# Optimization experiments

Measured on AMD Instinct MI355X. Metric: run time of the kernel, lower is better.

Reference implementation:

```python
import jax, jax.numpy as jnp
import numpy as np

TNEI = 2
TOPK = 4
NEIGH = 2 * TNEI + 1  # window size = 5


def _normalize(x, eps=1e-12):
    # matches torch F.normalize(dim=-1)
    n = jnp.linalg.norm(x, axis=-1, keepdims=True)
    return x / jnp.maximum(n, eps)


def setup_inputs() -> dict:
    key = jax.random.key(0)
    ks = jax.random.split(key, 10)
    B, T, C = 32, 256, 128
    x = jax.random.normal(ks[0], (B, T, C), jnp.float32)
    radj = jax.random.randint(ks[1], (B, T, T), 0, 2).astype(jnp.int32)
    inxs = jax.random.randint(ks[2], (B, T, TOPK), 0, T)
    s = 1.0 / np.sqrt(C)
    W_pf = jax.random.normal(ks[3], (C, C), jnp.float32) * s
    W_ns = jax.random.normal(ks[4], (C, C), jnp.float32) * s
    W_v = jax.random.normal(ks[5], (C, C), jnp.float32) * s
    v_pf = jax.random.normal(ks[6], (NEIGH,), jnp.float32)
    g_pf = jnp.linalg.norm(v_pf)[None]  # weight_norm gain, shape (1,)
    v_ns = jax.random.normal(ks[7], (TOPK,), jnp.float32)
    g_ns = jnp.linalg.norm(v_ns)[None]
    return dict(x=x, radj=radj, inxs=inxs, W_pf=W_pf, W_ns=W_ns, W_v=W_v,
                v_pf=v_pf, g_pf=g_pf, v_ns=v_ns, g_ns=g_ns)


def reference(x, radj, inxs, W_pf, W_ns, W_v, v_pf, g_pf, v_ns, g_ns):
    B, T, C = x.shape
    pf = _normalize(x @ W_pf.T)
    ns = _normalize(x @ W_ns.T)
    v = x @ W_v.T
    # windowed neighbor indices, identical to _tneigh_mask(mode='all')
    i = jnp.arange(T)
    start = jnp.clip(i - TNEI, 0, T - NEIGH)
    nbr = start[:, None] + jnp.arange(NEIGH)[None, :]  # (T, NEIGH)
    ctx = pf[:, nbr]  # (B, T, NEIGH, C) — replaces one-hot ctxinx einsum
    # pairwise window similarity: (B,T,T,n,n)
    sim = jnp.einsum('bxic,byjc->bxyij', ctx, ctx)
    # AdaptiveMaxPool2d((n,1)) == max over the last (key-window) axis
    sim_pf = sim.max(axis=-1)  # (B,T,T,n)
    w_pf = g_pf[0] * v_pf / jnp.linalg.norm(v_pf)  # weight-norm agg_pf
    sim_pf = jnp.einsum('bxyi,i->bxy', sim_pf, w_pf)
    # topk-neighbor branch: inxs gathers ns rows (replaces one-hot einsum)
    ns_q = ns[jnp.arange(B)[:, None, None], inxs]  # (B,T,TOPK,C)
    sim_ns = jnp.einsum('bxnc,byc->bxyn', ns_q, ns)  # (B,T,T,TOPK)
    w_ns = g_ns[0] * v_ns / jnp.linalg.norm(v_ns)  # weight-norm agg_ns
    sim_ns = jnp.einsum('bxyn,n->bxy', sim_ns, w_ns)
    # adjacency mask: 0 -> -1e22, >0 -> 0
    mask = jnp.where(radj == 0, jnp.float32(-1e22), jnp.float32(0.0))
    attn = jax.nn.softmax(sim_pf + sim_ns + mask, axis=-1)  # (B,T,T)
    return jnp.einsum('bkt,btd->bkd', attn, v)  # (B,T,C)
```

## Files before the change

kernel.cpp:

```cpp
#include <hip/hip_runtime.h>
#include <math.h>


#define TT 256
#define CC 128

using bf16x8 = __attribute__((ext_vector_type(8))) short;
using f32x4  = __attribute__((ext_vector_type(4))) float;

__device__ __forceinline__ short bf_hi(float x) {
    unsigned u = __float_as_uint(x);
    return (short)((u + 0x7FFFu + ((u >> 16) & 1u)) >> 16);
}
__device__ __forceinline__ void bf_split(float x, short& h, short& l) {
    h = bf_hi(x);
    float hf = __uint_as_float(((unsigned)(unsigned short)h) << 16);
    l = bf_hi(x - hf);
}
__device__ __forceinline__ float max5(float a, float b, float c, float d, float e) {
    return fmaxf(fmaxf(fmaxf(a, b), fmaxf(c, d)), e);
}

__global__ __launch_bounds__(256, 4) void proj_kernel(
    const float* __restrict__ x,
    const float* __restrict__ W0, const float* __restrict__ W1, const float* __restrict__ W2,
    float* __restrict__ pf, float* __restrict__ ns,
    short* __restrict__ vt_h, short* __restrict__ vt_l)
{
    __shared__ short Ah[32 * 40], Al[32 * 40];
    __shared__ short Bh[128 * 40], Bl[128 * 40];
    __shared__ float ssb[32][4];
    const int tid = threadIdx.x;
    const int row0 = blockIdx.x * 32;
    const int m = blockIdx.y;
    const float* __restrict__ W = (m == 0) ? W0 : (m == 1) ? W1 : W2;
    const int lane = tid & 63, wn = tid >> 6;
    const int quad = lane >> 4, lr = lane & 15;
    f32x4 z4 = {0.f, 0.f, 0.f, 0.f};
    f32x4 acc[2][2] = {{z4, z4}, {z4, z4}};

    for (int k0 = 0; k0 < CC; k0 += 32) {
        __syncthreads();
        {
            int r = tid >> 3, q = (tid & 7) * 4;
            float4 a4 = *(const float4*)&x[(row0 + r) * CC + k0 + q];
            short4 h4, l4;
            bf_split(a4.x, h4.x, l4.x); bf_split(a4.y, h4.y, l4.y);
            bf_split(a4.z, h4.z, l4.z); bf_split(a4.w, h4.w, l4.w);
            *(short4*)&Ah[r * 40 + q] = h4; *(short4*)&Al[r * 40 + q] = l4;
        }
        for (int i = 0; i < 4; i++) {
            int flat = i * 256 + tid, r = flat >> 3, q = (flat & 7) * 4;
            float4 b4 = *(const float4*)&W[r * CC + k0 + q];
            short4 h4, l4;
            bf_split(b4.x, h4.x, l4.x); bf_split(b4.y, h4.y, l4.y);
            bf_split(b4.z, h4.z, l4.z); bf_split(b4.w, h4.w, l4.w);
            *(short4*)&Bh[r * 40 + q] = h4; *(short4*)&Bl[r * 40 + q] = l4;
        }
        __syncthreads();
        bf16x8 ah[2], al[2], bh[2], bl[2];
        for (int ra = 0; ra < 2; ra++) {
            int ar = (16 * ra + lr) * 40 + quad * 8;
            ah[ra] = *(bf16x8*)&Ah[ar];
            al[ra] = *(bf16x8*)&Al[ar];
        }
        for (int tn = 0; tn < 2; tn++) {
            int br = (32 * wn + 16 * tn + lr) * 40 + quad * 8;
            bh[tn] = *(bf16x8*)&Bh[br];
            bl[tn] = *(bf16x8*)&Bl[br];
        }
        for (int ra = 0; ra < 2; ra++)
            for (int tn = 0; tn < 2; tn++) {
                acc[ra][tn] = __builtin_amdgcn_mfma_f32_16x16x32_bf16(ah[ra], bh[tn], acc[ra][tn], 0, 0, 0);
                acc[ra][tn] = __builtin_amdgcn_mfma_f32_16x16x32_bf16(ah[ra], bl[tn], acc[ra][tn], 0, 0, 0);
                acc[ra][tn] = __builtin_amdgcn_mfma_f32_16x16x32_bf16(al[ra], bh[tn], acc[ra][tn], 0, 0, 0);
            }
    }
    if (m < 2) {
        float* __restrict__ o = (m == 0) ? pf : ns;
        float ssp[2][4];
        for (int ra = 0; ra < 2; ra++)
            for (int reg = 0; reg < 4; reg++) {
                float s = acc[ra][0][reg] * acc[ra][0][reg]
                        + acc[ra][1][reg] * acc[ra][1][reg];
                for (int off = 1; off < 16; off <<= 1) s += __shfl_xor(s, off);
                ssp[ra][reg] = s;
            }
        if (lr == 0)
            for (int ra = 0; ra < 2; ra++)
                for (int reg = 0; reg < 4; reg++)
                    ssb[16 * ra + quad * 4 + reg][wn] = ssp[ra][reg];
        __syncthreads();
        for (int ra = 0; ra < 2; ra++)
            for (int reg = 0; reg < 4; reg++) {
                int ml = 16 * ra + quad * 4 + reg;
                float ss = ssb[ml][0] + ssb[ml][1] + ssb[ml][2] + ssb[ml][3];
                float inv = 1.f / fmaxf(sqrtf(ss), 1e-12f);
                int row = row0 + ml;
                for (int tn = 0; tn < 2; tn++)
                    o[row * CC + 32 * wn + 16 * tn + lr] = acc[ra][tn][reg] * inv;
            }
    } else {
        for (int ra = 0; ra < 2; ra++) {
            int rowbase = row0 + 16 * ra + quad * 4;
            int b = rowbase >> 8, t0 = rowbase & 255;
            for (int tn = 0; tn < 2; tn++) {
                int c = 32 * wn + 16 * tn + lr;
                short4 h4, l4;
                for (int reg = 0; reg < 4; reg++)
                    bf_split(acc[ra][tn][reg], ((short*)&h4)[reg], ((short*)&l4)[reg]);
                size_t o = ((size_t)b * CC + c) * TT + t0;
                *(short4*)&vt_h[o] = h4;
                *(short4*)&vt_l[o] = l4;
            }
        }
    }
}

__global__ __launch_bounds__(256, 4) void gram_mfma(
    const float* __restrict__ pf, const float* __restrict__ ns,
    const int* __restrict__ inxs, const float* __restrict__ v_ns,
    const float* __restrict__ g_ns, float* __restrict__ G, float* __restrict__ S)
{
    __shared__ short Ah[64 * 40], Al[64 * 40], Bh[64 * 40], Bl[64 * 40];
    const int tid = threadIdx.x;
    const int m0 = blockIdx.x * 64, n0 = blockIdx.y * 64;
    const int b = blockIdx.z >> 1, half = blockIdx.z & 1;
    const float* __restrict__ Pb = pf + (size_t)b * TT * CC;
    const float* __restrict__ Nb = ns + (size_t)b * TT * CC;
    const float* __restrict__ Bsrc = half ? Nb : Pb;

    float w0 = 0.f, w1 = 0.f, w2 = 0.f, w3 = 0.f;
    int4 id0 = {0, 0, 0, 0}, id1 = {0, 0, 0, 0};
    if (half) {
        float n2 = v_ns[0]*v_ns[0] + v_ns[1]*v_ns[1] + v_ns[2]*v_ns[2] + v_ns[3]*v_ns[3];
        float sc = g_ns[0] / sqrtf(n2);
        w0 = sc*v_ns[0]; w1 = sc*v_ns[1]; w2 = sc*v_ns[2]; w3 = sc*v_ns[3];
        id0 = *(const int4*)&inxs[(b * TT + m0 + (tid >> 3)) * 4];
        id1 = *(const int4*)&inxs[(b * TT + m0 + 32 + (tid >> 3)) * 4];
    }

    const int lane = tid & 63, wave = tid >> 6;
    const int wm = wave >> 1, wn = wave & 1;
    const int quad = lane >> 4, lr = lane & 15;
    f32x4 z4 = {0.f, 0.f, 0.f, 0.f};
    f32x4 acc[2][2] = {{z4, z4}, {z4, z4}};

    for (int k0 = 0; k0 < CC; k0 += 32) {
        __syncthreads();
        for (int i = 0; i < 2; i++) {
            int flat = i * 256 + tid, r = flat >> 3, q = (flat & 7) * 4;
            float4 a4;
            if (!half) {
                a4 = *(const float4*)&Pb[(m0 + r) * CC + k0 + q];
            } else {
                int4 id = i ? id1 : id0;
                float4 aa = *(const float4*)&Nb[id.x * CC + k0 + q];
                float4 ab = *(const float4*)&Nb[id.y * CC + k0 + q];
                float4 ac = *(const float4*)&Nb[id.z * CC + k0 + q];
                float4 ad = *(const float4*)&Nb[id.w * CC + k0 + q];
                a4.x = w0*aa.x + w1*ab.x + w2*ac.x + w3*ad.x;
                a4.y = w0*aa.y + w1*ab.y + w2*ac.y + w3*ad.y;
                a4.z = w0*aa.z + w1*ab.z + w2*ac.z + w3*ad.z;
                a4.w = w0*aa.w + w1*ab.w + w2*ac.w + w3*ad.w;
            }
            float4 b4 = *(const float4*)&Bsrc[(n0 + r) * CC + k0 + q];
            short4 h4, l4;
            bf_split(a4.x, h4.x, l4.x); bf_split(a4.y, h4.y, l4.y);
            bf_split(a4.z, h4.z, l4.z); bf_split(a4.w, h4.w, l4.w);
            *(short4*)&Ah[r * 40 + q] = h4; *(short4*)&Al[r * 40 + q] = l4;
            bf_split(b4.x, h4.x, l4.x); bf_split(b4.y, h4.y, l4.y);
            bf_split(b4.z, h4.z, l4.z); bf_split(b4.w, h4.w, l4.w);
            *(short4*)&Bh[r * 40 + q] = h4; *(short4*)&Bl[r * 40 + q] = l4;
        }
        __syncthreads();
        bf16x8 bh[2], bl[2];
        for (int tn = 0; tn < 2; tn++) {
            int br = (32 * wn + 16 * tn + lr) * 40 + quad * 8;
            bh[tn] = *(bf16x8*)&Bh[br];
            bl[tn] = *(bf16x8*)&Bl[br];
        }
        for (int tm = 0; tm < 2; tm++) {
            int ar = (32 * wm + 16 * tm + lr) * 40 + quad * 8;
            bf16x8 ah = *(bf16x8*)&Ah[ar];
            bf16x8 al = *(bf16x8*)&Al[ar];
            for (int tn = 0; tn < 2; tn++) {
                acc[tm][tn] = __builtin_amdgcn_mfma_f32_16x16x32_bf16(ah, bh[tn], acc[tm][tn], 0, 0, 0);
                acc[tm][tn] = __builtin_amdgcn_mfma_f32_16x16x32_bf16(ah, bl[tn], acc[tm][tn], 0, 0, 0);
                acc[tm][tn] = __builtin_amdgcn_mfma_f32_16x16x32_bf16(al, bh[tn], acc[tm][tn], 0, 0, 0);
            }
        }
    }
    float* __restrict__ Cb = (half ? S : G) + (size_t)b * TT * TT;
    for (int tm = 0; tm < 2; tm++)
        for (int tn = 0; tn < 2; tn++) {
            int rb = m0 + 32 * wm + 16 * tm + quad * 4;
            int cb = n0 + 32 * wn + 16 * tn + lr;
            for (int reg = 0; reg < 4; reg++)
                Cb[(size_t)(rb + reg) * TT + cb] = acc[tm][tn][reg];
        }
}

__global__ __launch_bounds__(256, 2) void fused_smax_pv(
    const float* __restrict__ G, const float* __restrict__ S,
    const int* __restrict__ radj, const float* __restrict__ v_pf,
    const float* __restrict__ g_pf,
    const short* __restrict__ vt_h, const short* __restrict__ vt_l,
    float* __restrict__ out)
{
    __shared__ float Gs[20 * 256];
    __shared__ float RM[20 * 256];
    __shared__ short ATH[16 * 264];
    __shared__ short ATL[16 * 264];
    __shared__ float RD[64];
    __shared__ float RMX[64];
    const int tid = threadIdx.x;
    const int xt = blockIdx.x, b = blockIdx.y;
    const int x0 = xt * 16;
    const int rbase = min(max(x0 - 2, 0), TT - 5);
    for (int i = 0; i < 5; i++) {
        int flat = i * 256 + tid, ri = flat >> 6, q = (flat & 63) * 4;
        int r = min(rbase + ri, TT - 1);
        *(float4*)&Gs[ri * 256 + q] = *(const float4*)&G[(size_t)b * TT * TT + r * TT + q];
    }
    float n2 = 0.f;
    for (int i = 0; i < 5; i++) n2 += v_pf[i] * v_pf[i];
    float sc = g_pf[0] / sqrtf(n2);
    float wpf[5];
    for (int i = 0; i < 5; i++) wpf[i] = sc * v_pf[i];
    __syncthreads();
    for (int t = 0; t < 5; t++) {
        int task = t * 256 + tid;
        int i = task >> 6, g = task & 63;
        const float* row = &Gs[i * 256];
        float4 X = *(float4*)&row[4 * g];
        float m0_, m1_, m2_, m3_;
        if (g == 0) {
            float4 N = *(float4*)&row[4];
            float mx = fmaxf(fmaxf(X.x, X.y), fmaxf(X.z, X.w));
            m0_ = m1_ = m2_ = fmaxf(mx, N.x);
            m3_ = max5(X.y, X.z, X.w, N.x, N.y);
        } else if (g == 63) {
            float4 P = *(float4*)&row[248];
            m0_ = max5(P.z, P.w, X.x, X.y, X.z);
            float mx = fmaxf(fmaxf(X.x, X.y), fmaxf(X.z, X.w));
            m1_ = m2_ = m3_ = fmaxf(P.w, mx);
        } else {
            float4 P = *(float4*)&row[4 * g - 4];
            float4 N = *(float4*)&row[4 * g + 4];
            m0_ = max5(P.z, P.w, X.x, X.y, X.z);
            m1_ = max5(P.w, X.x, X.y, X.z, X.w);
            m2_ = max5(X.x, X.y, X.z, X.w, N.x);
            m3_ = max5(X.y, X.z, X.w, N.x, N.y);
        }
        float4 o4 = {m0_, m1_, m2_, m3_};
        *(float4*)&RM[i * 256 + 4 * g] = o4;
    }
    __syncthreads();
    const int y = tid;
    const size_t sb = (size_t)b * TT * TT;
    float lv[16];
    if (xt > 0 && xt < 15) {
        float rm[20];
        #pragma unroll
        for (int r = 0; r < 20; r++) rm[r] = RM[r * 256 + y];
        #pragma unroll
        for (int xi = 0; xi < 16; xi++) {
            float s = wpf[0] * rm[xi];
            #pragma unroll
            for (int i = 1; i < 5; i++) s = fmaf(wpf[i], rm[xi + i], s);
            lv[xi] = s;
        }
    } else {
        for (int xi = 0; xi < 16; xi++) {
            int sxr = min(max(x0 + xi - 2, 0), TT - 5) - rbase;
            float s = 0.f;
            for (int i = 0; i < 5; i++) s = fmaf(wpf[i], RM[(sxr + i) * 256 + y], s);
            lv[xi] = s;
        }
    }
    for (int xi = 0; xi < 16; xi++) {
        lv[xi] += S[sb + (x0 + xi) * TT + y];
        if (radj[sb + (x0 + xi) * TT + y] == 0) lv[xi] += -1e22f;
    }
    const int lane = tid & 63, wv = tid >> 6;
    for (int xi = 0; xi < 16; xi++) {
        float v = lv[xi];
        for (int o = 32; o; o >>= 1) v = fmaxf(v, __shfl_xor(v, o));
        if (lane == 0) RMX[xi * 4 + wv] = v;
    }
    __syncthreads();
    for (int xi = 0; xi < 16; xi++) {
        float mx = fmaxf(fmaxf(RMX[xi * 4], RMX[xi * 4 + 1]),
                         fmaxf(RMX[xi * 4 + 2], RMX[xi * 4 + 3]));
        float e = __expf(lv[xi] - mx);
        short h, l;
        bf_split(e, h, l);
        ATH[xi * 264 + y] = h;
        ATL[xi * 264 + y] = l;
        for (int o = 32; o; o >>= 1) e += __shfl_xor(e, o);
        if (lane == 0) RD[xi * 4 + wv] = e;
    }
    __syncthreads();
    const int quad = lane >> 4, lr = lane & 15;
    const int c0 = wv * 32;
    const short* __restrict__ vhb = vt_h + (size_t)b * CC * TT;
    const short* __restrict__ vlb = vt_l + (size_t)b * CC * TT;
    const int ar0 = (c0 + lr) * TT, ar1 = ar0 + 16 * TT;
    f32x4 z4 = {0.f, 0.f, 0.f, 0.f};
    f32x4 acc[2] = {z4, z4};
    #pragma unroll
    for (int k0 = 0; k0 < TT; k0 += 32) {
        int ko = k0 + quad * 8;
        bf16x8 bh = *(bf16x8*)&ATH[lr * 264 + ko];
        bf16x8 bl = *(bf16x8*)&ATL[lr * 264 + ko];
        bf16x8 a0h = *(const bf16x8*)&vhb[ar0 + ko];
        bf16x8 a0l = *(const bf16x8*)&vlb[ar0 + ko];
        bf16x8 a1h = *(const bf16x8*)&vhb[ar1 + ko];
        bf16x8 a1l = *(const bf16x8*)&vlb[ar1 + ko];
        acc[0] = __builtin_amdgcn_mfma_f32_16x16x32_bf16(a0h, bh, acc[0], 0, 0, 0);
        acc[0] = __builtin_amdgcn_mfma_f32_16x16x32_bf16(a0h, bl, acc[0], 0, 0, 0);
        acc[0] = __builtin_amdgcn_mfma_f32_16x16x32_bf16(a0l, bh, acc[0], 0, 0, 0);
        acc[1] = __builtin_amdgcn_mfma_f32_16x16x32_bf16(a1h, bh, acc[1], 0, 0, 0);
        acc[1] = __builtin_amdgcn_mfma_f32_16x16x32_bf16(a1h, bl, acc[1], 0, 0, 0);
        acc[1] = __builtin_amdgcn_mfma_f32_16x16x32_bf16(a1l, bh, acc[1], 0, 0, 0);
    }
    float sm = RD[lr * 4] + RD[lr * 4 + 1] + RD[lr * 4 + 2] + RD[lr * 4 + 3];
    float rinv = 1.f / sm;
    for (int tm = 0; tm < 2; tm++) {
        float4 r;
        r.x = acc[tm][0] * rinv; r.y = acc[tm][1] * rinv;
        r.z = acc[tm][2] * rinv; r.w = acc[tm][3] * rinv;
        *(float4*)&out[(size_t)b * TT * CC + (x0 + lr) * CC + c0 + 16 * tm + quad * 4] = r;
    }
}

extern "C" void kernel_launch(void* const* d_in, const int* in_sizes, int n_in,
                              void* d_out, int out_size, void* d_ws, size_t ws_size,
                              hipStream_t stream) {
    const float* x    = (const float*)d_in[0];
    const int*   radj = (const int*)d_in[1];
    const int*   inxs = (const int*)d_in[2];
    const float* Wpf  = (const float*)d_in[3];
    const float* Wns  = (const float*)d_in[4];
    const float* Wv   = (const float*)d_in[5];
    const float* v_pf = (const float*)d_in[6];
    const float* g_pf = (const float*)d_in[7];
    const float* v_ns = (const float*)d_in[8];
    const float* g_ns = (const float*)d_in[9];
    float* out = (float*)d_out;

    char* base = (char*)d_ws;
    float* pf   = (float*)(base);
    float* ns   = (float*)(base + (4u << 20));
    short* vt_h = (short*)(base + (8u << 20));
    short* vt_l = (short*)(base + (10u << 20));
    float* G    = (float*)(base + (12u << 20));
    float* S    = (float*)(base + (20u << 20));

    proj_kernel<<<dim3(256, 3), 256, 0, stream>>>(x, Wpf, Wns, Wv, pf, ns, vt_h, vt_l);
    gram_mfma<<<dim3(4, 4, 64), 256, 0, stream>>>(pf, ns, inxs, v_ns, g_ns, G, S);
    fused_smax_pv<<<dim3(16, 32), 256, 0, stream>>>(G, S, radj, v_pf, g_pf,
                                                    vt_h, vt_l, out);
}
```

Baseline: 126.6 us.

## Fuse gram computation into softmax-PV kernel and store pf/ns as split bf16

Removes the separate gram kernel and the G/S intermediate matrices in global memory. Each block now computes its own window rows of the pf Gram tile and the ns-query similarity tile with MFMA straight from global pre-split bf16 hi/lo data, then runs softmax and PV as before. proj_kernel writes pf and ns already split into bf16 hi/lo pairs, so the splitting no longer has to be redone on load. In exchange, each block recomputes 32 overlapping Gram rows against all 256 columns, issues many uncoalesced global loads without LDS staging, and carries more accumulator registers, which may limit occupancy.

Result: no change. 127.6 us (+0.8%).

```diff
diff --git a/kernel.cpp b/kernel.cpp
--- a/kernel.cpp
+++ b/kernel.cpp
@@ -17,6 +17,9 @@
     float hf = __uint_as_float(((unsigned)(unsigned short)h) << 16);
     l = bf_hi(x - hf);
 }
+__device__ __forceinline__ float bf2f(short h) {
+    return __uint_as_float(((unsigned)(unsigned short)h) << 16);
+}
 __device__ __forceinline__ float max5(float a, float b, float c, float d, float e) {
     return fmaxf(fmaxf(fmaxf(a, b), fmaxf(c, d)), e);
 }
@@ -24,7 +27,8 @@
 __global__ __launch_bounds__(256, 4) void proj_kernel(
     const float* __restrict__ x,
     const float* __restrict__ W0, const float* __restrict__ W1, const float* __restrict__ W2,
-    float* __restrict__ pf, float* __restrict__ ns,
+    short* __restrict__ pf_h, short* __restrict__ pf_l,
+    short* __restrict__ ns_h, short* __restrict__ ns_l,
     short* __restrict__ vt_h, short* __restrict__ vt_l)
 {
     __shared__ short Ah[32 * 40], Al[32 * 40];
@@ -77,7 +81,8 @@
             }
     }
     if (m < 2) {
-        float* __restrict__ o = (m == 0) ? pf : ns;
+        short* __restrict__ oh = (m == 0) ? pf_h : ns_h;
+        short* __restrict__ ol = (m == 0) ? pf_l : ns_l;
         float ssp[2][4];
         for (int ra = 0; ra < 2; ra++)
             for (int reg = 0; reg < 4; reg++) {
@@ -97,8 +102,13 @@
                 float ss = ssb[ml][0] + ssb[ml][1] + ssb[ml][2] + ssb[ml][3];
                 float inv = 1.f / fmaxf(sqrtf(ss), 1e-12f);
                 int row = row0 + ml;
-                for (int tn = 0; tn < 2; tn++)
-                    o[row * CC + 32 * wn + 16 * tn + lr] = acc[ra][tn][reg] * inv;
+                for (int tn = 0; tn < 2; tn++) {
+                    float v = acc[ra][tn][reg] * inv;
+                    short h, l;
+                    bf_split(v, h, l);
+                    int idx = row * CC + 32 * wn + 16 * tn + lr;
+                    oh[idx] = h; ol[idx] = l;
+                }
             }
     } else {
         for (int ra = 0; ra < 2; ra++) {
@@ -117,122 +127,106 @@
     }
 }
 
-__global__ __launch_bounds__(256, 4) void gram_mfma(
-    const float* __restrict__ pf, const float* __restrict__ ns,
+__global__ __launch_bounds__(256, 2) void bigfused(
+    const short* __restrict__ pf_h, const short* __restrict__ pf_l,
+    const short* __restrict__ ns_h, const short* __restrict__ ns_l,
     const int* __restrict__ inxs, const float* __restrict__ v_ns,
-    const float* __restrict__ g_ns, float* __restrict__ G, float* __restrict__ S)
-{
-    __shared__ short Ah[64 * 40], Al[64 * 40], Bh[64 * 40], Bl[64 * 40];
-    const int tid = threadIdx.x;
-    const int m0 = blockIdx.x * 64, n0 = blockIdx.y * 64;
-    const int b = blockIdx.z >> 1, half = blockIdx.z & 1;
-    const float* __restrict__ Pb = pf + (size_t)b * TT * CC;
-    const float* __restrict__ Nb = ns + (size_t)b * TT * CC;
-    const float* __restrict__ Bsrc = half ? Nb : Pb;
-
-    float w0 = 0.f, w1 = 0.f, w2 = 0.f, w3 = 0.f;
-    int4 id0 = {0, 0, 0, 0}, id1 = {0, 0, 0, 0};
-    if (half) {
-        float n2 = v_ns[0]*v_ns[0] + v_ns[1]*v_ns[1] + v_ns[2]*v_ns[2] + v_ns[3]*v_ns[3];
-        float sc = g_ns[0] / sqrtf(n2);
-        w0 = sc*v_ns[0]; w1 = sc*v_ns[1]; w2 = sc*v_ns[2]; w3 = sc*v_ns[3];
-        id0 = *(const int4*)&inxs[(b * TT + m0 + (tid >> 3)) * 4];
-        id1 = *(const int4*)&inxs[(b * TT + m0 + 32 + (tid >> 3)) * 4];
-    }
-
-    const int lane = tid & 63, wave = tid >> 6;
-    const int wm = wave >> 1, wn = wave & 1;
-    const int quad = lane >> 4, lr = lane & 15;
-    f32x4 z4 = {0.f, 0.f, 0.f, 0.f};
-    f32x4 acc[2][2] = {{z4, z4}, {z4, z4}};
-
-    for (int k0 = 0; k0 < CC; k0 += 32) {
-        __syncthreads();
-        for (int i = 0; i < 2; i++) {
-            int flat = i * 256 + tid, r = flat >> 3, q = (flat & 7) * 4;
-            float4 a4;
-            if (!half) {
-                a4 = *(const float4*)&Pb[(m0 + r) * CC + k0 + q];
-            } else {
-                int4 id = i ? id1 : id0;
-                float4 aa = *(const float4*)&Nb[id.x * CC + k0 + q];
-                float4 ab = *(const float4*)&Nb[id.y * CC + k0 + q];
-                float4 ac = *(const float4*)&Nb[id.z * CC + k0 + q];
-                float4 ad = *(const float4*)&Nb[id.w * CC + k0 + q];
-                a4.x = w0*aa.x + w1*ab.x + w2*ac.x + w3*ad.x;
-                a4.y = w0*aa.y + w1*ab.y + w2*ac.y + w3*ad.y;
-                a4.z = w0*aa.z + w1*ab.z + w2*ac.z + w3*ad.z;
-                a4.w = w0*aa.w + w1*ab.w + w2*ac.w + w3*ad.w;
-            }
-            float4 b4 = *(const float4*)&Bsrc[(n0 + r) * CC + k0 + q];
-            short4 h4, l4;
-            bf_split(a4.x, h4.x, l4.x); bf_split(a4.y, h4.y, l4.y);
-            bf_split(a4.z, h4.z, l4.z); bf_split(a4.w, h4.w, l4.w);
-            *(short4*)&Ah[r * 40 + q] = h4; *(short4*)&Al[r * 40 + q] = l4;
-            bf_split(b4.x, h4.x, l4.x); bf_split(b4.y, h4.y, l4.y);
-            bf_split(b4.z, h4.z, l4.z); bf_split(b4.w, h4.w, l4.w);
-            *(short4*)&Bh[r * 40 + q] = h4; *(short4*)&Bl[r * 40 + q] = l4;
-        }
-        __syncthreads();
-        bf16x8 bh[2], bl[2];
-        for (int tn = 0; tn < 2; tn++) {
-            int br = (32 * wn + 16 * tn + lr) * 40 + quad * 8;
-            bh[tn] = *(bf16x8*)&Bh[br];
-            bl[tn] = *(bf16x8*)&Bl[br];
-        }
-        for (int tm = 0; tm < 2; tm++) {
-            int ar = (32 * wm + 16 * tm + lr) * 40 + quad * 8;
-            bf16x8 ah = *(bf16x8*)&Ah[ar];
-            bf16x8 al = *(bf16x8*)&Al[ar];
-            for (int tn = 0; tn < 2; tn++) {
-                acc[tm][tn] = __builtin_amdgcn_mfma_f32_16x16x32_bf16(ah, bh[tn], acc[tm][tn], 0, 0, 0);
-                acc[tm][tn] = __builtin_amdgcn_mfma_f32_16x16x32_bf16(ah, bl[tn], acc[tm][tn], 0, 0, 0);
-                acc[tm][tn] = __builtin_amdgcn_mfma_f32_16x16x32_bf16(al, bh[tn], acc[tm][tn], 0, 0, 0);
-            }
-        }
-    }
-    float* __restrict__ Cb = (half ? S : G) + (size_t)b * TT * TT;
-    for (int tm = 0; tm < 2; tm++)
-        for (int tn = 0; tn < 2; tn++) {
-            int rb = m0 + 32 * wm + 16 * tm + quad * 4;
-            int cb = n0 + 32 * wn + 16 * tn + lr;
-            for (int reg = 0; reg < 4; reg++)
-                Cb[(size_t)(rb + reg) * TT + cb] = acc[tm][tn][reg];
-        }
-}
-
-__global__ __launch_bounds__(256, 2) void fused_smax_pv(
-    const float* __restrict__ G, const float* __restrict__ S,
-    const int* __restrict__ radj, const float* __restrict__ v_pf,
-    const float* __restrict__ g_pf,
+    const float* __restrict__ g_ns, const int* __restrict__ radj,
+    const float* __restrict__ v_pf, const float* __restrict__ g_pf,
     const short* __restrict__ vt_h, const short* __restrict__ vt_l,
     float* __restrict__ out)
 {
-    __shared__ float Gs[20 * 256];
-    __shared__ float RM[20 * 256];
-    __shared__ short ATH[16 * 264];
-    __shared__ short ATL[16 * 264];
-    __shared__ float RD[64];
-    __shared__ float RMX[64];
+    __shared__ float lds[14336];
+    float* Gb  = &lds[0];
+    float* Sb  = &lds[5120];
+    float* RM  = &lds[9216];
+    short* ATH = (short*)&lds[0];
+    short* ATL = (short*)&lds[2112];
+    float* RD  = &lds[4224];
+    float* RMX = &lds[4288];
+
     const int tid = threadIdx.x;
     const int xt = blockIdx.x, b = blockIdx.y;
     const int x0 = xt * 16;
     const int rbase = min(max(x0 - 2, 0), TT - 5);
-    for (int i = 0; i < 5; i++) {
-        int flat = i * 256 + tid, ri = flat >> 6, q = (flat & 63) * 4;
-        int r = min(rbase + ri, TT - 1);
-        *(float4*)&Gs[ri * 256 + q] = *(const float4*)&G[(size_t)b * TT * TT + r * TT + q];
-    }
-    float n2 = 0.f;
-    for (int i = 0; i < 5; i++) n2 += v_pf[i] * v_pf[i];
-    float sc = g_pf[0] / sqrtf(n2);
-    float wpf[5];
-    for (int i = 0; i < 5; i++) wpf[i] = sc * v_pf[i];
+    const int a0 = min(rbase, TT - 32);
+    const int d = rbase - a0;
+    const size_t nb = (size_t)b * TT * CC;
+    const int lane = tid & 63, w = tid >> 6;
+    const int quad = lane >> 4, lr = lane & 15;
+
+    bf16x8 aqh[4], aql[4];
+    {
+        float n2 = v_ns[0]*v_ns[0] + v_ns[1]*v_ns[1] + v_ns[2]*v_ns[2] + v_ns[3]*v_ns[3];
+        float sc = g_ns[0] / sqrtf(n2);
+        float wq[4] = {sc*v_ns[0], sc*v_ns[1], sc*v_ns[2], sc*v_ns[3]};
+        int4 id = *(const int4*)&inxs[(b * TT + x0 + lr) * 4];
+        int idl[4] = {id.x, id.y, id.z, id.w};
+        float qv[4][8] = {};
+        for (int n = 0; n < 4; n++) {
+            const short* hb = &ns_h[nb + idl[n] * CC];
+            const short* lb = &ns_l[nb + idl[n] * CC];
+            for (int kk = 0; kk < 4; kk++) {
+                int ko = kk * 32 + quad * 8;
+                bf16x8 h8 = *(const bf16x8*)&hb[ko];
+                bf16x8 l8 = *(const bf16x8*)&lb[ko];
+                for (int e = 0; e < 8; e++)
+                    qv[kk][e] = fmaf(wq[n], bf2f(h8[e]) + bf2f(l8[e]), qv[kk][e]);
+            }
+        }
+        for (int kk = 0; kk < 4; kk++)
+            for (int e = 0; e < 8; e++)
+                bf_split(qv[kk][e], ((short*)&aqh[kk])[e], ((short*)&aql[kk])[e]);
+    }
+
+    const int am0 = (a0 + lr) * CC, am1 = am0 + 16 * CC;
+    int bcol[4];
+    for (int c = 0; c < 4; c++) bcol[c] = (c * 64 + w * 16 + lr) * CC;
+    f32x4 z4 = {0.f, 0.f, 0.f, 0.f};
+    f32x4 accg[2][4], accs[4];
+    for (int tm = 0; tm < 2; tm++) for (int c = 0; c < 4; c++) accg[tm][c] = z4;
+    for (int c = 0; c < 4; c++) accs[c] = z4;
+
+    #pragma unroll
+    for (int kk = 0; kk < 4; kk++) {
+        int ko = kk * 32 + quad * 8;
+        bf16x8 a0h = *(const bf16x8*)&pf_h[nb + am0 + ko];
+        bf16x8 a0l = *(const bf16x8*)&pf_l[nb + am0 + ko];
+        bf16x8 a1h = *(const bf16x8*)&pf_h[nb + am1 + ko];
+        bf16x8 a1l = *(const bf16x8*)&pf_l[nb + am1 + ko];
+        #pragma unroll
+        for (int c = 0; c < 4; c++) {
+            bf16x8 bph = *(const bf16x8*)&pf_h[nb + bcol[c] + ko];
+            bf16x8 bpl = *(const bf16x8*)&pf_l[nb + bcol[c] + ko];
+            bf16x8 bnh = *(const bf16x8*)&ns_h[nb + bcol[c] + ko];
+            bf16x8 bnl = *(const bf16x8*)&ns_l[nb + bcol[c] + ko];
+            accg[0][c] = __builtin_amdgcn_mfma_f32_16x16x32_bf16(a0h, bph, accg[0][c], 0, 0, 0);
+            accg[0][c] = __builtin_amdgcn_mfma_f32_16x16x32_bf16(a0h, bpl, accg[0][c], 0, 0, 0);
+            accg[0][c] = __builtin_amdgcn_mfma_f32_16x16x32_bf16(a0l, bph, accg[0][c], 0, 0, 0);
+            accg[1][c] = __builtin_amdgcn_mfma_f32_16x16x32_bf16(a1h, bph, accg[1][c], 0, 0, 0);
+            accg[1][c] = __builtin_amdgcn_mfma_f32_16x16x32_bf16(a1h, bpl, accg[1][c], 0, 0, 0);
+            accg[1][c] = __builtin_amdgcn_mfma_f32_16x16x32_bf16(a1l, bph, accg[1][c], 0, 0, 0);
+            accs[c]    = __builtin_amdgcn_mfma_f32_16x16x32_bf16(aqh[kk], bnh, accs[c], 0, 0, 0);
+            accs[c]    = __builtin_amdgcn_mfma_f32_16x16x32_bf16(aqh[kk], bnl, accs[c], 0, 0, 0);
+            accs[c]    = __builtin_amdgcn_mfma_f32_16x16x32_bf16(aql[kk], bnh, accs[c], 0, 0, 0);
+        }
+    }
+    for (int tm = 0; tm < 2; tm++)
+        for (int c = 0; c < 4; c++)
+            for (int reg = 0; reg < 4; reg++) {
+                int gr = 16 * tm + quad * 4 + reg;
+                if (gr >= d && gr < d + 20)
+                    Gb[(gr - d) * 256 + c * 64 + w * 16 + lr] = accg[tm][c][reg];
+            }
+    for (int c = 0; c < 4; c++)
+        for (int reg = 0; reg < 4; reg++)
+            Sb[(quad * 4 + reg) * 256 + c * 64 + w * 16 + lr] = accs[c][reg];
     __syncthreads();
+
     for (int t = 0; t < 5; t++) {
         int task = t * 256 + tid;
         int i = task >> 6, g = task & 63;
-        const float* row = &Gs[i * 256];
+        const float* row = &Gb[min(i, 31 - d) * 256];
         float4 X = *(float4*)&row[4 * g];
         float m0_, m1_, m2_, m3_;
         if (g == 0) {
@@ -257,6 +251,12 @@
         *(float4*)&RM[i * 256 + 4 * g] = o4;
     }
     __syncthreads();
+
+    float n2p = 0.f;
+    for (int i = 0; i < 5; i++) n2p += v_pf[i] * v_pf[i];
+    float scp = g_pf[0] / sqrtf(n2p);
+    float wpf[5];
+    for (int i = 0; i < 5; i++) wpf[i] = scp * v_pf[i];
     const int y = tid;
     const size_t sb = (size_t)b * TT * TT;
     float lv[16];
@@ -280,14 +280,13 @@
         }
     }
     for (int xi = 0; xi < 16; xi++) {
-        lv[xi] += S[sb + (x0 + xi) * TT + y];
+        lv[xi] += Sb[xi * 256 + y];
         if (radj[sb + (x0 + xi) * TT + y] == 0) lv[xi] += -1e22f;
     }
-    const int lane = tid & 63, wv = tid >> 6;
     for (int xi = 0; xi < 16; xi++) {
         float v = lv[xi];
         for (int o = 32; o; o >>= 1) v = fmaxf(v, __shfl_xor(v, o));
-        if (lane == 0) RMX[xi * 4 + wv] = v;
+        if (lane == 0) RMX[xi * 4 + w] = v;
     }
     __syncthreads();
     for (int xi = 0; xi < 16; xi++) {
@@ -299,16 +298,15 @@
         ATH[xi * 264 + y] = h;
         ATL[xi * 264 + y] = l;
         for (int o = 32; o; o >>= 1) e += __shfl_xor(e, o);
-        if (lane == 0) RD[xi * 4 + wv] = e;
+        if (lane == 0) RD[xi * 4 + w] = e;
     }
     __syncthreads();
-    const int quad = lane >> 4, lr = lane & 15;
-    const int c0 = wv * 32;
+
+    const int c0 = w * 32;
     const short* __restrict__ vhb = vt_h + (size_t)b * CC * TT;
     const short* __restrict__ vlb = vt_l + (size_t)b * CC * TT;
     const int ar0 = (c0 + lr) * TT, ar1 = ar0 + 16 * TT;
-    f32x4 z4 = {0.f, 0.f, 0.f, 0.f};
-    f32x4 acc[2] = {z4, z4};
+    f32x4 acc2[2] = {z4, z4};
     #pragma unroll
     for (int k0 = 0; k0 < TT; k0 += 32) {
         int ko = k0 + quad * 8;
@@ -318,19 +316,19 @@
         bf16x8 a0l = *(const bf16x8*)&vlb[ar0 + ko];
         bf16x8 a1h = *(const bf16x8*)&vhb[ar1 + ko];
         bf16x8 a1l = *(const bf16x8*)&vlb[ar1 + ko];
-        acc[0] = __builtin_amdgcn_mfma_f32_16x16x32_bf16(a0h, bh, acc[0], 0, 0, 0);
-        acc[0] = __builtin_amdgcn_mfma_f32_16x16x32_bf16(a0h, bl, acc[0], 0, 0, 0);
-        acc[0] = __builtin_amdgcn_mfma_f32_16x16x32_bf16(a0l, bh, acc[0], 0, 0, 0);
-        acc[1] = __builtin_amdgcn_mfma_f32_16x16x32_bf16(a1h, bh, acc[1], 0, 0, 0);
-        acc[1] = __builtin_amdgcn_mfma_f32_16x16x32_bf16(a1h, bl, acc[1], 0, 0, 0);
-        acc[1] = __builtin_amdgcn_mfma_f32_16x16x32_bf16(a1l, bh, acc[1], 0, 0, 0);
+        acc2[0] = __builtin_amdgcn_mfma_f32_16x16x32_bf16(a0h, bh, acc2[0], 0, 0, 0);
+        acc2[0] = __builtin_amdgcn_mfma_f32_16x16x32_bf16(a0h, bl, acc2[0], 0, 0, 0);
+        acc2[0] = __builtin_amdgcn_mfma_f32_16x16x32_bf16(a0l, bh, acc2[0], 0, 0, 0);
+        acc2[1] = __builtin_amdgcn_mfma_f32_16x16x32_bf16(a1h, bh, acc2[1], 0, 0, 0);
+        acc2[1] = __builtin_amdgcn_mfma_f32_16x16x32_bf16(a1h, bl, acc2[1], 0, 0, 0);
+        acc2[1] = __builtin_amdgcn_mfma_f32_16x16x32_bf16(a1l, bh, acc2[1], 0, 0, 0);
     }
     float sm = RD[lr * 4] + RD[lr * 4 + 1] + RD[lr * 4 + 2] + RD[lr * 4 + 3];
     float rinv = 1.f / sm;
     for (int tm = 0; tm < 2; tm++) {
         float4 r;
-        r.x = acc[tm][0] * rinv; r.y = acc[tm][1] * rinv;
-        r.z = acc[tm][2] * rinv; r.w = acc[tm][3] * rinv;
+        r.x = acc2[tm][0] * rinv; r.y = acc2[tm][1] * rinv;
+        r.z = acc2[tm][2] * rinv; r.w = acc2[tm][3] * rinv;
         *(float4*)&out[(size_t)b * TT * CC + (x0 + lr) * CC + c0 + 16 * tm + quad * 4] = r;
     }
 }
@@ -351,15 +349,16 @@
     float* out = (float*)d_out;
 
     char* base = (char*)d_ws;
-    float* pf   = (float*)(base);
-    float* ns   = (float*)(base + (4u << 20));
+    short* pf_h = (short*)(base);
+    short* pf_l = (short*)(base + (2u << 20));
+    short* ns_h = (short*)(base + (4u << 20));
+    short* ns_l = (short*)(base + (6u << 20));
     short* vt_h = (short*)(base + (8u << 20));
     short* vt_l = (short*)(base + (10u << 20));
-    float* G    = (float*)(base + (12u << 20));
-    float* S    = (float*)(base + (20u << 20));
-
-    proj_kernel<<<dim3(256, 3), 256, 0, stream>>>(x, Wpf, Wns, Wv, pf, ns, vt_h, vt_l);
-    gram_mfma<<<dim3(4, 4, 64), 256, 0, stream>>>(pf, ns, inxs, v_ns, g_ns, G, S);
-    fused_smax_pv<<<dim3(16, 32), 256, 0, stream>>>(G, S, radj, v_pf, g_pf,
-                                                    vt_h, vt_l, out);
-}
+
+    proj_kernel<<<dim3(256, 3), 256, 0, stream>>>(x, Wpf, Wns, Wv,
+                                                  pf_h, pf_l, ns_h, ns_l, vt_h, vt_l);
+    bigfused<<<dim3(16, 32), 256, 0, stream>>>(pf_h, pf_l, ns_h, ns_l,
+                                               inxs, v_ns, g_ns, radj, v_pf, g_pf,
+                                               vt_h, vt_l, out);
+}
```
